# Kernel optimization log

Measured on AMD Instinct MI355X. Metric: run time of the kernel, lower is better.

Reference implementation:

```python
import jax, jax.numpy as jnp
import numpy as np
import math

B, S, HID = 2, 1024, 2048
NH, HD = 16, 128
STREAM_R, SELECT_R, RECENT_R = 0.02, 0.06, 0.08
FF = 0.9  # forgetting factor
ROPE_BASE = 10000.0


def setup_inputs() -> dict:
    key = jax.random.key(0)
    ks = jax.random.split(key, 5)
    return {
        "hidden_states": jax.random.normal(ks[0], (B, S, HID), dtype=jnp.float32),
        "wq": jax.random.normal(ks[1], (HID, HID), dtype=jnp.float32) * 0.02,
        "wk": jax.random.normal(ks[2], (HID, HID), dtype=jnp.float32) * 0.02,
        "wv": jax.random.normal(ks[3], (HID, HID), dtype=jnp.float32) * 0.02,
        "wo": jax.random.normal(ks[4], (HID, HID), dtype=jnp.float32) * 0.02,
    }


def _rope_tables(seq_len, dim):
    inv_freq = 1.0 / (ROPE_BASE ** (jnp.arange(0, dim, 2, dtype=jnp.float32) / dim))
    freqs = jnp.outer(jnp.arange(seq_len, dtype=jnp.float32), inv_freq)  # [S, D/2]
    emb = jnp.concatenate([freqs, freqs], axis=-1)  # [S, D]
    return jnp.cos(emb), jnp.sin(emb)


def _rotate_half(x):
    x1, x2 = jnp.split(x, 2, axis=-1)
    return jnp.concatenate([-x2, x1], axis=-1)


def a2s_base_mask(attn_weights, sb, selb, rb, ff):
    # attn_weights: [B,H,S,S] (causal mask already added). Returns bool keep-mask [B,H,S,S].
    Bv, Hv, Sq, Sk = attn_weights.shape
    scores = jax.nn.softmax(attn_weights.astype(jnp.float32), axis=-1)  # [B,H,S,S]
    cb = sb + selb + rb  # cache budget
    # EMA warmup over first cb rows: sum_i ff^(cb-1-i) * scores[i]
    w = ff ** jnp.arange(cb - 1, -1, -1, dtype=jnp.float32)
    select0 = jnp.einsum('t,bhts->bhs', w, scores[:, :, :cb, :])
    mask0 = jnp.ones((Bv, Hv, Sk), dtype=bool)
    pos = jnp.arange(Sk)

    xs_scores = jnp.moveaxis(scores[:, :, cb:Sk - 1, :], 2, 0)  # [T,B,H,S]
    ts = jnp.arange(cb, Sk - 1, dtype=jnp.int32)

    def step(carry, inp):
        sel, m = carry
        sc, t = inp
        cur = sc * m
        cur = cur / jnp.sum(cur, axis=-1, keepdims=True)
        sel = ff * sel + cur
        local = t - rb
        # argmin over window [sb : local+1]; outside -> +inf (evicted entries already +inf)
        win = jnp.where((pos >= sb) & (pos <= local), sel, jnp.inf)
        mi = jnp.argmin(win, axis=-1)  # [B,H], first-min like torch
        evict = pos == mi[..., None]  # [B,H,S] one-hot bool
        sel = jnp.where(evict, jnp.inf, sel)
        m_new = m & ~evict
        return (sel, m_new), m_new

    _, rows = jax.lax.scan(step, (select0, mask0), (xs_scores, ts))
    head = jnp.ones((Bv, Hv, cb + 1, Sk), dtype=bool)  # rows 0..cb stay all-True
    tail = jnp.moveaxis(rows, 0, 2)  # rows cb+1..S-1
    return jnp.concatenate([head, tail], axis=2)


def reference(hidden_states, wq, wk, wv, wo):
    sb = math.floor(STREAM_R * S + 0.5)
    selb = math.floor(SELECT_R * S + 0.5)
    rb = math.floor(RECENT_R * S + 0.5)

    q = (hidden_states @ wq).reshape(B, S, NH, HD).transpose(0, 2, 1, 3)
    k = (hidden_states @ wk).reshape(B, S, NH, HD).transpose(0, 2, 1, 3)
    v = (hidden_states @ wv).reshape(B, S, NH, HD).transpose(0, 2, 1, 3)

    cos, sin = _rope_tables(S, HD)  # [S,HD]
    q = q * cos + _rotate_half(q) * sin
    k = k * cos + _rotate_half(k) * sin

    attn = jnp.einsum('bhqd,bhkd->bhqk', q, k) / math.sqrt(HD)
    mask_val = jnp.finfo(jnp.float32).min
    causal = jnp.where(jnp.tril(jnp.ones((S, S), dtype=bool)), 0.0, mask_val)[None, None]
    attn = jnp.maximum(attn + causal, mask_val)

    keep = a2s_base_mask(jax.lax.stop_gradient(attn), sb, selb, rb, FF)
    attn = jnp.where(keep, attn, mask_val)  # torch.min(attention_mask) == mask_val

    probs = jax.nn.softmax(attn.astype(jnp.float32), axis=-1).astype(q.dtype)
    out = jnp.einsum('bhqk,bhkd->bhqd', probs, v)
    out = out.transpose(0, 2, 1, 3).reshape(B, S, HID)
    return out @ wo
```

## Files before the change

### kernel.cpp

```cpp
#include <hip/hip_runtime.h>
#include <math.h>

#define Bb    2
#define Ss    1024
#define HIDd  2048
#define NHh   16
#define HDd   128
#define SBc   20
#define SELBc 61
#define RBc   82
#define CBc   163
#define FFf   0.9f
#define MASKVAL (-3.4028234663852886e38f)
#define NBH   (Bb*NHh)
#define NROWS (NBH*Ss)

typedef __attribute__((ext_vector_type(8))) short short8;
typedef __attribute__((ext_vector_type(4))) float f32x4;

__device__ __forceinline__ unsigned short f2b(float f) {
    unsigned u = __float_as_uint(f);
    u = (u + 0x7FFFu + ((u >> 16) & 1u)) >> 16;
    return (unsigned short)u;
}
__device__ __forceinline__ float b2f(unsigned short h) {
    return __uint_as_float((unsigned)h << 16);
}

__global__ __launch_bounds__(256) void conv_split(const float* __restrict__ x,
                                                  unsigned short* __restrict__ yh,
                                                  unsigned short* __restrict__ yl, int n4)
{
    int i = blockIdx.x * 256 + threadIdx.x;
    if (i >= n4) return;
    float4 v = ((const float4*)x)[i];
    ushort4 h, l;
    h.x = f2b(v.x); l.x = f2b(v.x - b2f(h.x));
    h.y = f2b(v.y); l.y = f2b(v.y - b2f(h.y));
    h.z = f2b(v.z); l.z = f2b(v.z - b2f(h.z));
    h.w = f2b(v.w); l.w = f2b(v.w - b2f(h.w));
    ((ushort4*)yh)[i] = h;
    ((ushort4*)yl)[i] = l;
}

__global__ __launch_bounds__(256) void tconv(const float* __restrict__ W,
                                             unsigned short* __restrict__ Wt,
                                             int Kdim, int Ndim)
{
    __shared__ float T[64][65];
    int n0 = blockIdx.x * 64, k0 = blockIdx.y * 64;
    int tid = threadIdx.x;
    int rr = tid >> 4, cc = (tid & 15) * 4;
#pragma unroll
    for (int p = 0; p < 4; ++p) {
        int r = rr + p * 16;
        float4 x = *(const float4*)&W[(size_t)(k0 + r) * Ndim + n0 + cc];
        T[r][cc] = x.x; T[r][cc + 1] = x.y; T[r][cc + 2] = x.z; T[r][cc + 3] = x.w;
    }
    __syncthreads();
#pragma unroll
    for (int p = 0; p < 4; ++p) {
        int rn = rr + p * 16;
        ushort4 o;
        o.x = f2b(T[cc][rn]);     o.y = f2b(T[cc + 1][rn]);
        o.z = f2b(T[cc + 2][rn]); o.w = f2b(T[cc + 3][rn]);
        *(ushort4*)&Wt[(size_t)(n0 + rn) * Kdim + k0 + cc] = o;
    }
}

__global__ __launch_bounds__(256) void tconv_split(const float* __restrict__ W,
                                                   unsigned short* __restrict__ Wth,
                                                   unsigned short* __restrict__ Wtl,
                                                   int Kdim, int Ndim)
{
    __shared__ float T[64][65];
    int n0 = blockIdx.x * 64, k0 = blockIdx.y * 64;
    int tid = threadIdx.x;
    int rr = tid >> 4, cc = (tid & 15) * 4;
#pragma unroll
    for (int p = 0; p < 4; ++p) {
        int r = rr + p * 16;
        float4 x = *(const float4*)&W[(size_t)(k0 + r) * Ndim + n0 + cc];
        T[r][cc] = x.x; T[r][cc + 1] = x.y; T[r][cc + 2] = x.z; T[r][cc + 3] = x.w;
    }
    __syncthreads();
#pragma unroll
    for (int p = 0; p < 4; ++p) {
        int rn = rr + p * 16;
        float v0 = T[cc][rn], v1 = T[cc + 1][rn], v2 = T[cc + 2][rn], v3 = T[cc + 3][rn];
        ushort4 h, l;
        h.x = f2b(v0); l.x = f2b(v0 - b2f(h.x));
        h.y = f2b(v1); l.y = f2b(v1 - b2f(h.y));
        h.z = f2b(v2); l.z = f2b(v2 - b2f(h.z));
        h.w = f2b(v3); l.w = f2b(v3 - b2f(h.w));
        *(ushort4*)&Wth[(size_t)(n0 + rn) * Kdim + k0 + cc] = h;
        *(ushort4*)&Wtl[(size_t)(n0 + rn) * Kdim + k0 + cc] = l;
    }
}

template<int MODE>
__global__ __launch_bounds__(256) void gemm_bf16t(const unsigned short* __restrict__ A,
                                                  const unsigned short* __restrict__ Bt,
                                                  float* __restrict__ C,
                                                  int M, int N, int K)
{
    __shared__ unsigned short As[128 * 32];
    __shared__ unsigned short Bs[128 * 32];
    const int tid = threadIdx.x;
    const int bm = blockIdx.y * 128, bn = blockIdx.x * 128;
    const int lane = tid & 63, wid = tid >> 6;
    const int wr = (wid >> 1) * 64, wc = (wid & 1) * 64;
    const int lm = lane & 15, lk = (lane >> 4) * 8;

    f32x4 acc[4][4];
#pragma unroll
    for (int mi = 0; mi < 4; ++mi)
#pragma unroll
        for (int ni = 0; ni < 4; ++ni) acc[mi][ni] = 0.0f;

    for (int k0 = 0; k0 < K; k0 += 32) {
#pragma unroll
        for (int l = 0; l < 2; ++l) {
            int L = tid + l * 256;
            int row = L >> 2, c8 = (L & 3) * 8;
            *(short8*)&As[row * 32 + c8] = *(const short8*)&A[(size_t)(bm + row) * K + k0 + c8];
            *(short8*)&Bs[row * 32 + c8] = *(const short8*)&Bt[(size_t)(bn + row) * K + k0 + c8];
        }
        __syncthreads();
        short8 af[4], bf[4];
#pragma unroll
        for (int mi = 0; mi < 4; ++mi) af[mi] = *(short8*)&As[(wr + mi * 16 + lm) * 32 + lk];
#pragma unroll
        for (int ni = 0; ni < 4; ++ni) bf[ni] = *(short8*)&Bs[(wc + ni * 16 + lm) * 32 + lk];
#pragma unroll
        for (int mi = 0; mi < 4; ++mi)
#pragma unroll
            for (int ni = 0; ni < 4; ++ni)
                acc[mi][ni] = __builtin_amdgcn_mfma_f32_16x16x32_bf16(af[mi], bf[ni], acc[mi][ni], 0, 0, 0);
        __syncthreads();
    }
    const int lr = (lane >> 4) * 4;
#pragma unroll
    for (int mi = 0; mi < 4; ++mi)
#pragma unroll
        for (int ni = 0; ni < 4; ++ni)
#pragma unroll
            for (int r = 0; r < 4; ++r) {
                int m = bm + wr + mi * 16 + lr + r;
                int n = bn + wc + ni * 16 + lm;
                float vv = acc[mi][ni][r];
                if (MODE == 0) {
                    C[(size_t)m * N + n] = vv;
                } else {
                    int b_ = m / Ss, s_ = m % Ss;
                    int h_ = n / HDd, d_ = n % HDd;
                    C[(size_t)((b_ * NHh + h_) * Ss + s_) * HDd + d_] = vv;
                }
            }
}

template<int MODE>
__global__ __launch_bounds__(256) void gemm_split(const unsigned short* __restrict__ Ah,
                                                  const unsigned short* __restrict__ Al,
                                                  const unsigned short* __restrict__ Bh,
                                                  const unsigned short* __restrict__ Bl,
                                                  float* __restrict__ C,
                                                  int M, int N, int K)
{
    __shared__ unsigned short AsH[128 * 32], AsL[128 * 32];
    __shared__ unsigned short BsH[128 * 32], BsL[128 * 32];
    const int tid = threadIdx.x;
    const int bm = blockIdx.y * 128, bn = blockIdx.x * 128;
    const int lane = tid & 63, wid = tid >> 6;
    const int wr = (wid >> 1) * 64, wc = (wid & 1) * 64;
    const int lm = lane & 15, lk = (lane >> 4) * 8;

    f32x4 acc[4][4];
#pragma unroll
    for (int mi = 0; mi < 4; ++mi)
#pragma unroll
        for (int ni = 0; ni < 4; ++ni) acc[mi][ni] = 0.0f;

    for (int k0 = 0; k0 < K; k0 += 32) {
#pragma unroll
        for (int l = 0; l < 2; ++l) {
            int L = tid + l * 256;
            int row = L >> 2, c8 = (L & 3) * 8;
            size_t ga = (size_t)(bm + row) * K + k0 + c8;
            size_t gb = (size_t)(bn + row) * K + k0 + c8;
            *(short8*)&AsH[row * 32 + c8] = *(const short8*)&Ah[ga];
            *(short8*)&AsL[row * 32 + c8] = *(const short8*)&Al[ga];
            *(short8*)&BsH[row * 32 + c8] = *(const short8*)&Bh[gb];
            *(short8*)&BsL[row * 32 + c8] = *(const short8*)&Bl[gb];
        }
        __syncthreads();
        short8 ah[4], al[4], bh[4], bl[4];
#pragma unroll
        for (int mi = 0; mi < 4; ++mi) {
            ah[mi] = *(short8*)&AsH[(wr + mi * 16 + lm) * 32 + lk];
            al[mi] = *(short8*)&AsL[(wr + mi * 16 + lm) * 32 + lk];
        }
#pragma unroll
        for (int ni = 0; ni < 4; ++ni) {
            bh[ni] = *(short8*)&BsH[(wc + ni * 16 + lm) * 32 + lk];
            bl[ni] = *(short8*)&BsL[(wc + ni * 16 + lm) * 32 + lk];
        }
#pragma unroll
        for (int mi = 0; mi < 4; ++mi)
#pragma unroll
            for (int ni = 0; ni < 4; ++ni) {
                acc[mi][ni] = __builtin_amdgcn_mfma_f32_16x16x32_bf16(ah[mi], bh[ni], acc[mi][ni], 0, 0, 0);
                acc[mi][ni] = __builtin_amdgcn_mfma_f32_16x16x32_bf16(ah[mi], bl[ni], acc[mi][ni], 0, 0, 0);
                acc[mi][ni] = __builtin_amdgcn_mfma_f32_16x16x32_bf16(al[mi], bh[ni], acc[mi][ni], 0, 0, 0);
            }
        __syncthreads();
    }
    const int lr = (lane >> 4) * 4;
#pragma unroll
    for (int mi = 0; mi < 4; ++mi)
#pragma unroll
        for (int ni = 0; ni < 4; ++ni)
#pragma unroll
            for (int r = 0; r < 4; ++r) {
                int m = bm + wr + mi * 16 + lr + r;
                int n = bn + wc + ni * 16 + lm;
                float vv = acc[mi][ni][r];
                if (MODE == 0) {
                    C[(size_t)m * N + n] = vv;
                } else {
                    int b_ = m / Ss, s_ = m % Ss;
                    int h_ = n / HDd, d_ = n % HDd;
                    C[(size_t)((b_ * NHh + h_) * Ss + s_) * HDd + d_] = vv;
                }
            }
}

__global__ __launch_bounds__(64) void rope_qk_split(const float* __restrict__ q,
                                                    const float* __restrict__ k,
                                                    unsigned short* __restrict__ qh,
                                                    unsigned short* __restrict__ ql,
                                                    unsigned short* __restrict__ kh,
                                                    unsigned short* __restrict__ kl)
{
    int idx = blockIdx.x;
    int s = idx % Ss;
    int d = threadIdx.x;
    float inv = powf(10000.0f, -2.0f * (float)d / 128.0f);
    float fr = (float)s * inv;
    float c = cosf(fr), sn = sinf(fr);
    size_t base = (size_t)idx * HDd;
    float q1 = q[base + d], q2 = q[base + d + 64];
    float k1 = k[base + d], k2 = k[base + d + 64];
    float qa = q1 * c - q2 * sn, qbv = q2 * c + q1 * sn;
    float ka = k1 * c - k2 * sn, kbv = k2 * c + k1 * sn;
    unsigned short h;
    h = f2b(qa);  qh[base + d]      = h; ql[base + d]      = f2b(qa  - b2f(h));
    h = f2b(qbv); qh[base + d + 64] = h; ql[base + d + 64] = f2b(qbv - b2f(h));
    h = f2b(ka);  kh[base + d]      = h; kl[base + d]      = f2b(ka  - b2f(h));
    h = f2b(kbv); kh[base + d + 64] = h; kl[base + d + 64] = f2b(kbv - b2f(h));
}

__global__ __launch_bounds__(256) void attn_qk_split(const unsigned short* __restrict__ qh,
                                                     const unsigned short* __restrict__ ql,
                                                     const unsigned short* __restrict__ kh,
                                                     const unsigned short* __restrict__ kl,
                                                     float* __restrict__ attn)
{
    const int bh = blockIdx.z;
    const int bm = blockIdx.y * 128, bn = blockIdx.x * 128;
    float* C = attn + (size_t)bh * Ss * Ss;
    const int tid = threadIdx.x;

    if (blockIdx.x > blockIdx.y) {
        float4 mv = make_float4(MASKVAL, MASKVAL, MASKVAL, MASKVAL);
#pragma unroll
        for (int i = 0; i < 16; ++i) {
            int L = tid + i * 256;
            int row = L >> 5, c4 = (L & 31) * 4;
            *(float4*)&C[(size_t)(bm + row) * Ss + bn + c4] = mv;
        }
        return;
    }
    const size_t hb = (size_t)bh * Ss * HDd;
    const unsigned short* Ah = qh + hb;
    const unsigned short* Al = ql + hb;
    const unsigned short* Bh = kh + hb;
    const unsigned short* Bl = kl + hb;

    __shared__ unsigned short AsH[128 * 32], AsL[128 * 32];
    __shared__ unsigned short BsH[128 * 32], BsL[128 * 32];
    const int lane = tid & 63, wid = tid >> 6;
    const int wr = (wid >> 1) * 64, wc = (wid & 1) * 64;
    const int lm = lane & 15, lk = (lane >> 4) * 8;

    f32x4 acc[4][4];
#pragma unroll
    for (int mi = 0; mi < 4; ++mi)
#pragma unroll
        for (int ni = 0; ni < 4; ++ni) acc[mi][ni] = 0.0f;

    for (int k0 = 0; k0 < HDd; k0 += 32) {
#pragma unroll
        for (int l = 0; l < 2; ++l) {
            int L = tid + l * 256;
            int row = L >> 2, c8 = (L & 3) * 8;
            size_t ga = (size_t)(bm + row) * HDd + k0 + c8;
            size_t gb = (size_t)(bn + row) * HDd + k0 + c8;
            *(short8*)&AsH[row * 32 + c8] = *(const short8*)&Ah[ga];
            *(short8*)&AsL[row * 32 + c8] = *(const short8*)&Al[ga];
            *(short8*)&BsH[row * 32 + c8] = *(const short8*)&Bh[gb];
            *(short8*)&BsL[row * 32 + c8] = *(const short8*)&Bl[gb];
        }
        __syncthreads();
        short8 ah[4], al[4], bh2[4], bl2[4];
#pragma unroll
        for (int mi = 0; mi < 4; ++mi) {
            ah[mi] = *(short8*)&AsH[(wr + mi * 16 + lm) * 32 + lk];
            al[mi] = *(short8*)&AsL[(wr + mi * 16 + lm) * 32 + lk];
        }
#pragma unroll
        for (int ni = 0; ni < 4; ++ni) {
            bh2[ni] = *(short8*)&BsH[(wc + ni * 16 + lm) * 32 + lk];
            bl2[ni] = *(short8*)&BsL[(wc + ni * 16 + lm) * 32 + lk];
        }
#pragma unroll
        for (int mi = 0; mi < 4; ++mi)
#pragma unroll
            for (int ni = 0; ni < 4; ++ni) {
                acc[mi][ni] = __builtin_amdgcn_mfma_f32_16x16x32_bf16(ah[mi], bh2[ni], acc[mi][ni], 0, 0, 0);
                acc[mi][ni] = __builtin_amdgcn_mfma_f32_16x16x32_bf16(ah[mi], bl2[ni], acc[mi][ni], 0, 0, 0);
                acc[mi][ni] = __builtin_amdgcn_mfma_f32_16x16x32_bf16(al[mi], bh2[ni], acc[mi][ni], 0, 0, 0);
            }
        __syncthreads();
    }
    const float scale = 0.08838834764831845f;
    const int lr = (lane >> 4) * 4;
#pragma unroll
    for (int mi = 0; mi < 4; ++mi)
#pragma unroll
        for (int ni = 0; ni < 4; ++ni)
#pragma unroll
            for (int r = 0; r < 4; ++r) {
                int sq = bm + wr + mi * 16 + lr + r;
                int sk = bn + wc + ni * 16 + lm;
                C[(size_t)sq * Ss + sk] = (sk <= sq) ? acc[mi][ni][r] * scale : MASKVAL;
            }
}

__global__ __launch_bounds__(256) void softmax_rows(float* __restrict__ attn)
{
    int row = blockIdx.x;
    float4* a4 = (float4*)(attn + (size_t)row * Ss);
    int tid = threadIdx.x;
    float4 x = a4[tid];
    float m = fmaxf(fmaxf(x.x, x.y), fmaxf(x.z, x.w));
#pragma unroll
    for (int off = 32; off; off >>= 1) m = fmaxf(m, __shfl_xor(m, off));
    __shared__ float red[4];
    if ((tid & 63) == 0) red[tid >> 6] = m;
    __syncthreads();
    float mm = fmaxf(fmaxf(red[0], red[1]), fmaxf(red[2], red[3]));
    float e0 = expf(x.x - mm), e1 = expf(x.y - mm);
    float e2 = expf(x.z - mm), e3 = expf(x.w - mm);
    float s = e0 + e1 + e2 + e3;
#pragma unroll
    for (int off = 32; off; off >>= 1) s += __shfl_xor(s, off);
    __shared__ float red2[4];
    if ((tid & 63) == 0) red2[tid >> 6] = s;
    __syncthreads();
    float inv = 1.0f / (red2[0] + red2[1] + red2[2] + red2[3]);
    a4[tid] = make_float4(e0 * inv, e1 * inv, e2 * inv, e3 * inv);
}

template<int CTRL>
__device__ __forceinline__ int dpp_i(int x) {
    return __builtin_amdgcn_update_dpp(0, x, CTRL, 0xF, 0xF, true);
}
__device__ __forceinline__ float wave_sum64(float x) {
    x += __int_as_float(dpp_i<0xB1>(__float_as_int(x)));
    x += __int_as_float(dpp_i<0x4E>(__float_as_int(x)));
    x += __int_as_float(dpp_i<0x141>(__float_as_int(x)));
    x += __int_as_float(dpp_i<0x140>(__float_as_int(x)));
    int xi = __float_as_int(x);
    float a = __int_as_float(__builtin_amdgcn_readlane(xi, 0));
    float b = __int_as_float(__builtin_amdgcn_readlane(xi, 16));
    float c = __int_as_float(__builtin_amdgcn_readlane(xi, 32));
    float d = __int_as_float(__builtin_amdgcn_readlane(xi, 48));
    return (a + c) + (b + d);
}

__device__ __forceinline__ unsigned long long u64min(unsigned long long a, unsigned long long b) {
    return a < b ? a : b;
}
template<int CTRL>
__device__ __forceinline__ unsigned long long dpp64(unsigned long long x) {
    int lo = (int)(unsigned)x;
    int hi = (int)(unsigned)(x >> 32);
    unsigned l2 = (unsigned)dpp_i<CTRL>(lo);
    unsigned h2 = (unsigned)dpp_i<CTRL>(hi);
    return ((unsigned long long)h2 << 32) | (unsigned long long)l2;
}
__device__ __forceinline__ unsigned long long wave_min64k(unsigned long long x) {
    x = u64min(x, dpp64<0xB1>(x));
    x = u64min(x, dpp64<0x4E>(x));
    x = u64min(x, dpp64<0x141>(x));
    x = u64min(x, dpp64<0x140>(x));
    int lo = (int)(unsigned)x;
    int hi = (int)(unsigned)(x >> 32);
    unsigned long long a = ((unsigned long long)(unsigned)__builtin_amdgcn_readlane(hi, 0)  << 32) |
                           (unsigned long long)(unsigned)__builtin_amdgcn_readlane(lo, 0);
    unsigned long long b = ((unsigned long long)(unsigned)__builtin_amdgcn_readlane(hi, 16) << 32) |
                           (unsigned long long)(unsigned)__builtin_amdgcn_readlane(lo, 16);
    unsigned long long c = ((unsigned long long)(unsigned)__builtin_amdgcn_readlane(hi, 32) << 32) |
                           (unsigned long long)(unsigned)__builtin_amdgcn_readlane(lo, 32);
    unsigned long long d = ((unsigned long long)(unsigned)__builtin_amdgcn_readlane(hi, 48) << 32) |
                           (unsigned long long)(unsigned)__builtin_amdgcn_readlane(lo, 48);
    return u64min(u64min(a, b), u64min(c, d));
}

__device__ __forceinline__ float f4c(float4 v, int i) {
    return i == 0 ? v.x : (i == 1 ? v.y : (i == 2 ? v.z : v.w));
}

template<int NC, int NCL>
__device__ __forceinline__ void scan_step(int t, int lane,
                                          const float4* __restrict__ A4,
                                          unsigned char* __restrict__ KP,
                                          float4 (&rb)[4],
                                          float (&sel)[4][4],
                                          float (&mf)[4][4])
{
    const float INFv = __int_as_float(0x7f800000);
    float4 a[NC];
#pragma unroll
    for (int jj = 0; jj < NC; ++jj) a[jj] = rb[jj];
    int tp = t + 4; if (tp > Ss - 1) tp = Ss - 1;
#pragma unroll
    for (int jj = 0; jj < NCL; ++jj) rb[jj] = A4[tp * 256 + jj * 64 + lane];

    float lsum = 0.0f;
#pragma unroll
    for (int jj = 0; jj < NC; ++jj) {
        float c0 = a[jj].x * mf[jj][0], c1 = a[jj].y * mf[jj][1];
        float c2 = a[jj].z * mf[jj][2], c3 = a[jj].w * mf[jj][3];
        lsum += (c0 + c1) + (c2 + c3);
    }
    float tot = wave_sum64(lsum);
    float inv = 1.0f / tot;

    const int local = t - RBc;
    const int base = lane * 4;
    const bool ge = (base >= SBc);

    unsigned long long kmin = 0xFFFFFFFFFFFFFFFFull;
#pragma unroll
    for (int jj = 0; jj < NC; ++jj) {
        unsigned long long kk[4];
#pragma unroll
        for (int i = 0; i < 4; ++i) {
            float sv = fmaf(FFf, sel[jj][i], f4c(a[jj], i) * inv);
            sel[jj][i] = sv;
            int s = jj * 256 + base + i;
            bool win = (s <= local) && (jj > 0 || ge);
            unsigned hi = win ? __float_as_uint(sv) : 0x7f800000u;
            kk[i] = ((unsigned long long)hi << 32) | (unsigned long long)(unsigned)s;
        }
        unsigned long long cm = u64min(u64min(kk[0], kk[1]), u64min(kk[2], kk[3]));
        kmin = u64min(kmin, cm);
    }
    kmin = wave_min64k(kmin);
    const int besti = (int)(unsigned)(kmin & 0xFFFFFFFFull);

#pragma unroll
    for (int jj = 0; jj < NC; ++jj)
#pragma unroll
        for (int i = 0; i < 4; ++i) {
            int s = jj * 256 + base + i;
            bool e = (s == besti);
            sel[jj][i] = e ? INFv : sel[jj][i];
            mf[jj][i]  = e ? 0.0f : mf[jj][i];
        }

    uchar4* kp4 = (uchar4*)(KP + (size_t)(t + 1) * Ss);
#pragma unroll
    for (int jj = 0; jj < NC; ++jj) {
        uchar4 kb;
        kb.x = (unsigned char)mf[jj][0];
        kb.y = (unsigned char)mf[jj][1];
        kb.z = (unsigned char)mf[jj][2];
        kb.w = (unsigned char)mf[jj][3];
        kp4[jj * 64 + lane] = kb;
    }
}

__global__ __launch_bounds__(64) void scan_kernel5(const float* __restrict__ scores,
                                                   unsigned char* __restrict__ keep)
{
    int bh = blockIdx.x;
    int lane = threadIdx.x;
    const float4* A4 = (const float4*)(scores + (size_t)bh * Ss * Ss);
    unsigned char* KP = keep + (size_t)bh * Ss * Ss;

    float sel[4][4];
    float mf[4][4];
#pragma unroll
    for (int jj = 0; jj < 4; ++jj)
#pragma unroll
        for (int i = 0; i < 4; ++i) { sel[jj][i] = 0.0f; mf[jj][i] = 1.0f; }

    float4 w0 = A4[0 * 256 + lane];
    float4 w1 = A4[1 * 256 + lane];
    float4 w2 = A4[2 * 256 + lane];
    float4 w3 = A4[3 * 256 + lane];
#define WSTEP(W, NEXT)                                                       \
    do {                                                                     \
        float4 _a = W;                                                       \
        W = A4[(NEXT) * 256 + lane];                                         \
        sel[0][0] = fmaf(FFf, sel[0][0], _a.x);                              \
        sel[0][1] = fmaf(FFf, sel[0][1], _a.y);                              \
        sel[0][2] = fmaf(FFf, sel[0][2], _a.z);                              \
        sel[0][3] = fmaf(FFf, sel[0][3], _a.w);                              \
    } while (0)
    for (int r = 0; r < 160; r += 4) {
        WSTEP(w0, r + 4); WSTEP(w1, r + 5); WSTEP(w2, r + 6); WSTEP(w3, r + 7);
    }
#undef WSTEP
    {
        float4 tl[3] = { w0, w1, w2 };
#pragma unroll
        for (int u = 0; u < 3; ++u) {
            sel[0][0] = fmaf(FFf, sel[0][0], tl[u].x);
            sel[0][1] = fmaf(FFf, sel[0][1], tl[u].y);
            sel[0][2] = fmaf(FFf, sel[0][2], tl[u].z);
            sel[0][3] = fmaf(FFf, sel[0][3], tl[u].w);
        }
    }

    float4 rb[4][4];
#pragma unroll
    for (int slot = 0; slot < 4; ++slot)
        rb[slot][0] = A4[(163 + slot) * 256 + lane];

    for (int t0 = 163; t0 < 255; t0 += 4) {
        scan_step<1, 2>(t0 + 0, lane, A4, KP, rb[0], sel, mf);
        scan_step<1, 2>(t0 + 1, lane, A4, KP, rb[1], sel, mf);
        scan_step<1, 2>(t0 + 2, lane, A4, KP, rb[2], sel, mf);
        scan_step<1, 2>(t0 + 3, lane, A4, KP, rb[3], sel, mf);
    }
    for (int t0 = 255; t0 < 511; t0 += 4) {
        scan_step<2, 3>(t0 + 0, lane, A4, KP, rb[0], sel, mf);
        scan_step<2, 3>(t0 + 1, lane, A4, KP, rb[1], sel, mf);
        scan_step<2, 3>(t0 + 2, lane, A4, KP, rb[2], sel, mf);
        scan_step<2, 3>(t0 + 3, lane, A4, KP, rb[3], sel, mf);
    }
    for (int t0 = 511; t0 < 767; t0 += 4) {
        scan_step<3, 4>(t0 + 0, lane, A4, KP, rb[0], sel, mf);
        scan_step<3, 4>(t0 + 1, lane, A4, KP, rb[1], sel, mf);
        scan_step<3, 4>(t0 + 2, lane, A4, KP, rb[2], sel, mf);
        scan_step<3, 4>(t0 + 3, lane, A4, KP, rb[3], sel, mf);
    }
    for (int t0 = 767; t0 < 1023; t0 += 4) {
        scan_step<4, 4>(t0 + 0, lane, A4, KP, rb[0], sel, mf);
        scan_step<4, 4>(t0 + 1, lane, A4, KP, rb[1], sel, mf);
        scan_step<4, 4>(t0 + 2, lane, A4, KP, rb[2], sel, mf);
        scan_step<4, 4>(t0 + 3, lane, A4, KP, rb[3], sel, mf);
    }
}

__global__ __launch_bounds__(256) void renorm_rows(float* __restrict__ scores,
                                                   const unsigned char* __restrict__ keep)
{
    int row = blockIdx.x;
    int r = row % Ss;
    float4* a4 = (float4*)(scores + (size_t)row * Ss);
    int tid = threadIdx.x;
    float4 x = a4[tid];
    if (r > CBc) {
        const uchar4* kp = (const uchar4*)(keep + (size_t)row * Ss);
        uchar4 kb = kp[tid];
        if (!kb.x) x.x = 0.0f;
        if (!kb.y) x.y = 0.0f;
        if (!kb.z) x.z = 0.0f;
        if (!kb.w) x.w = 0.0f;
    }
    float s = (x.x + x.y) + (x.z + x.w);
#pragma unroll
    for (int off = 32; off; off >>= 1) s += __shfl_xor(s, off);
    __shared__ float red2[4];
    if ((tid & 63) == 0) red2[tid >> 6] = s;
    __syncthreads();
    float inv = 1.0f / (red2[0] + red2[1] + red2[2] + red2[3]);
    a4[tid] = make_float4(x.x * inv, x.y * inv, x.z * inv, x.w * inv);
}

__global__ __launch_bounds__(256) void pv_gemm(const float* __restrict__ probs,
                                               const float* __restrict__ v,
                                               unsigned short* __restrict__ ctxb)
{
    int bh = blockIdx.z;
    int b_ = bh / NHh, h_ = bh % NHh;
    const float* P = probs + (size_t)bh * Ss * Ss;
    const float* V = v     + (size_t)bh * Ss * HDd;
    int bm = blockIdx.y * 64, bn = blockIdx.x * 64;
    int tid = threadIdx.x, tx = tid & 15, ty = tid >> 4;
    __shared__ float As[16][65];
    __shared__ float Bs[16][64];
    float acc[4][4] = {};
    int kend = bm + 64;
    for (int k0 = 0; k0 < kend; k0 += 16) {
#pragma unroll
        for (int l = 0; l < 4; ++l) {
            int idx = tid + l * 256;
            int r = idx >> 4, c = idx & 15;
            As[c][r] = P[(size_t)(bm + r) * Ss + k0 + c];
        }
#pragma unroll
        for (int l = 0; l < 4; ++l) {
            int idx = tid + l * 256;
            int r = idx >> 6, c = idx & 63;
            Bs[r][c] = V[(size_t)(k0 + r) * HDd + bn + c];
        }
        __syncthreads();
#pragma unroll
        for (int kk = 0; kk < 16; ++kk) {
            float a[4], b[4];
#pragma unroll
            for (int i = 0; i < 4; ++i) a[i] = As[kk][ty * 4 + i];
#pragma unroll
            for (int j = 0; j < 4; ++j) b[j] = Bs[kk][tx * 4 + j];
#pragma unroll
            for (int i = 0; i < 4; ++i)
#pragma unroll
                for (int j = 0; j < 4; ++j)
                    acc[i][j] = fmaf(a[i], b[j], acc[i][j]);
        }
        __syncthreads();
    }
#pragma unroll
    for (int i = 0; i < 4; ++i) {
        int sq = bm + ty * 4 + i;
#pragma unroll
        for (int j = 0; j < 4; ++j) {
            int d = bn + tx * 4 + j;
            ctxb[(size_t)(b_ * Ss + sq) * HIDd + h_ * HDd + d] = f2b(acc[i][j]);
        }
    }
}

extern "C" void kernel_launch(void* const* d_in, const int* in_sizes, int n_in,
                              void* d_out, int out_size, void* d_ws, size_t ws_size,
                              hipStream_t stream)
{
    const float* hs = (const float*)d_in[0];
    const float* wq = (const float*)d_in[1];
    const float* wk = (const float*)d_in[2];
    const float* wv = (const float*)d_in[3];
    const float* wo = (const float*)d_in[4];
    float* out = (float*)d_out;

    float* ws = (float*)d_ws;
    size_t off = 0;
    float* qf   = ws + off; off += (size_t)NBH * Ss * HDd;
    float* kf   = ws + off; off += (size_t)NBH * Ss * HDd;
    float* vf   = ws + off; off += (size_t)NBH * Ss * HDd;
    float* attn = ws + off; off += (size_t)NBH * Ss * Ss;
    unsigned char* keep = (unsigned char*)(ws + off); off += (size_t)NBH * Ss * Ss / 4;
    unsigned short* wot = (unsigned short*)(ws + off); off += (size_t)HIDd * HIDd / 2;

    unsigned short* hsh  = (unsigned short*)(attn);
    unsigned short* hsl  = (unsigned short*)(attn + 2u * 1024 * 1024);
    unsigned short* wqth = (unsigned short*)(attn + 4u * 1024 * 1024);
    unsigned short* wqtl = (unsigned short*)(attn + 6u * 1024 * 1024);
    unsigned short* wkth = (unsigned short*)(attn + 8u * 1024 * 1024);
    unsigned short* wktl = (unsigned short*)(attn + 10u * 1024 * 1024);
    unsigned short* wvt  = (unsigned short*)(attn + 12u * 1024 * 1024);
    unsigned short* qh = (unsigned short*)keep;
    unsigned short* ql = (unsigned short*)(keep + 8u * 1024 * 1024);
    unsigned short* kh = (unsigned short*)(keep + 16u * 1024 * 1024);
    unsigned short* kl = (unsigned short*)(keep + 24u * 1024 * 1024);
    unsigned short* ctxb = (unsigned short*)qf;

    dim3 blk(256);
    const int M = Bb * Ss;

    conv_split<<<dim3((M * HIDd / 4 + 255) / 256), blk, 0, stream>>>(hs, hsh, hsl, M * HIDd / 4);

    dim3 gt(HIDd / 64, HIDd / 64);
    tconv_split<<<gt, blk, 0, stream>>>(wq, wqth, wqtl, HIDd, HIDd);
    tconv_split<<<gt, blk, 0, stream>>>(wk, wkth, wktl, HIDd, HIDd);
    tconv<<<gt, blk, 0, stream>>>(wv, wvt, HIDd, HIDd);
    tconv<<<gt, blk, 0, stream>>>(wo, wot, HIDd, HIDd);

    dim3 gp(HIDd / 128, M / 128);
    gemm_split<1><<<gp, blk, 0, stream>>>(hsh, hsl, wqth, wqtl, qf, M, HIDd, HIDd);
    gemm_split<1><<<gp, blk, 0, stream>>>(hsh, hsl, wkth, wktl, kf, M, HIDd, HIDd);
    gemm_bf16t<1><<<gp, blk, 0, stream>>>(hsh, wvt, vf, M, HIDd, HIDd);

    rope_qk_split<<<dim3(NBH * Ss), dim3(64), 0, stream>>>(qf, kf, qh, ql, kh, kl);

    attn_qk_split<<<dim3(Ss / 128, Ss / 128, NBH), blk, 0, stream>>>(qh, ql, kh, kl, attn);

    softmax_rows<<<dim3(NROWS), blk, 0, stream>>>(attn);

    scan_kernel5<<<dim3(NBH), dim3(64), 0, stream>>>(attn, keep);

    renorm_rows<<<dim3(NROWS), blk, 0, stream>>>(attn, keep);

    pv_gemm<<<dim3(HDd / 64, Ss / 64, NBH), blk, 0, stream>>>(attn, vf, ctxb);

    gemm_bf16t<0><<<gp, blk, 0, stream>>>(ctxb, wot, out, M, HIDd, HIDd);
}
```

Measured before the change: 1.040 ms.

## Fuse weight conversions, merge QKV GEMMs, fold renorm into PV, use direct LDS loads

Merges the four weight transpose/convert kernels into one launch and the Q, K and V projections into one grid. The upper-triangle mask fill in QK^T is dropped, and softmax now reads only the causal prefix of each row. The separate renorm pass is folded into the PV GEMM, which masks evicted keys on load and divides by the accumulated row sum. Tile loads switch to global_load_lds when the builtin is available. These target launch overhead and redundant passes over the S×S score matrix, with the risk that downstream code relies on the masked upper region no longer being written.

```diff
diff --git a/kernel.cpp b/kernel.cpp
--- a/kernel.cpp
+++ b/kernel.cpp
@@ -27,6 +27,22 @@
     return __uint_as_float((unsigned)h << 16);
 }
 
+#if defined(__has_builtin)
+#if __has_builtin(__builtin_amdgcn_global_load_lds)
+#define USE_GLD 1
+#endif
+#endif
+
+__device__ __forceinline__ void gload16(const void* g, void* l) {
+#ifdef USE_GLD
+    __builtin_amdgcn_global_load_lds(
+        (const __attribute__((address_space(1))) void*)g,
+        (__attribute__((address_space(3))) void*)l, 16, 0, 0);
+#else
+    *(short8*)l = *(const short8*)g;
+#endif
+}
+
 __global__ __launch_bounds__(256) void conv_split(const float* __restrict__ x,
                                                   unsigned short* __restrict__ yh,
                                                   unsigned short* __restrict__ yl, int n4)
@@ -43,62 +59,174 @@
     ((ushort4*)yl)[i] = l;
 }
 
-__global__ __launch_bounds__(256) void tconv(const float* __restrict__ W,
-                                             unsigned short* __restrict__ Wt,
-                                             int Kdim, int Ndim)
+__global__ __launch_bounds__(256) void tconv_all(const float* __restrict__ wq,
+                                                 const float* __restrict__ wk,
+                                                 const float* __restrict__ wv,
+                                                 const float* __restrict__ wo,
+                                                 unsigned short* __restrict__ wqth,
+                                                 unsigned short* __restrict__ wqtl,
+                                                 unsigned short* __restrict__ wkth,
+                                                 unsigned short* __restrict__ wktl,
+                                                 unsigned short* __restrict__ wvt,
+                                                 unsigned short* __restrict__ wot)
 {
     __shared__ float T[64][65];
+    const int z = blockIdx.z;
+    const float* W = (z == 0) ? wq : (z == 1) ? wk : (z == 2) ? wv : wo;
     int n0 = blockIdx.x * 64, k0 = blockIdx.y * 64;
     int tid = threadIdx.x;
     int rr = tid >> 4, cc = (tid & 15) * 4;
 #pragma unroll
     for (int p = 0; p < 4; ++p) {
         int r = rr + p * 16;
-        float4 x = *(const float4*)&W[(size_t)(k0 + r) * Ndim + n0 + cc];
+        float4 x = *(const float4*)&W[(size_t)(k0 + r) * HIDd + n0 + cc];
         T[r][cc] = x.x; T[r][cc + 1] = x.y; T[r][cc + 2] = x.z; T[r][cc + 3] = x.w;
     }
     __syncthreads();
-#pragma unroll
-    for (int p = 0; p < 4; ++p) {
-        int rn = rr + p * 16;
-        ushort4 o;
-        o.x = f2b(T[cc][rn]);     o.y = f2b(T[cc + 1][rn]);
-        o.z = f2b(T[cc + 2][rn]); o.w = f2b(T[cc + 3][rn]);
-        *(ushort4*)&Wt[(size_t)(n0 + rn) * Kdim + k0 + cc] = o;
-    }
-}
-
-__global__ __launch_bounds__(256) void tconv_split(const float* __restrict__ W,
-                                                   unsigned short* __restrict__ Wth,
-                                                   unsigned short* __restrict__ Wtl,
-                                                   int Kdim, int Ndim)
-{
-    __shared__ float T[64][65];
-    int n0 = blockIdx.x * 64, k0 = blockIdx.y * 64;
-    int tid = threadIdx.x;
-    int rr = tid >> 4, cc = (tid & 15) * 4;
-#pragma unroll
-    for (int p = 0; p < 4; ++p) {
-        int r = rr + p * 16;
-        float4 x = *(const float4*)&W[(size_t)(k0 + r) * Ndim + n0 + cc];
-        T[r][cc] = x.x; T[r][cc + 1] = x.y; T[r][cc + 2] = x.z; T[r][cc + 3] = x.w;
-    }
-    __syncthreads();
-#pragma unroll
-    for (int p = 0; p < 4; ++p) {
-        int rn = rr + p * 16;
-        float v0 = T[cc][rn], v1 = T[cc + 1][rn], v2 = T[cc + 2][rn], v3 = T[cc + 3][rn];
-        ushort4 h, l;
-        h.x = f2b(v0); l.x = f2b(v0 - b2f(h.x));
-        h.y = f2b(v1); l.y = f2b(v1 - b2f(h.y));
-        h.z = f2b(v2); l.z = f2b(v2 - b2f(h.z));
-        h.w = f2b(v3); l.w = f2b(v3 - b2f(h.w));
-        *(ushort4*)&Wth[(size_t)(n0 + rn) * Kdim + k0 + cc] = h;
-        *(ushort4*)&Wtl[(size_t)(n0 + rn) * Kdim + k0 + cc] = l;
-    }
-}
-
-template<int MODE>
+    if (z < 2) {
+        unsigned short* Wth = z ? wkth : wqth;
+        unsigned short* Wtl = z ? wktl : wqtl;
+#pragma unroll
+        for (int p = 0; p < 4; ++p) {
+            int rn = rr + p * 16;
+            float v0 = T[cc][rn], v1 = T[cc + 1][rn], v2 = T[cc + 2][rn], v3 = T[cc + 3][rn];
+            ushort4 h, l;
+            h.x = f2b(v0); l.x = f2b(v0 - b2f(h.x));
+            h.y = f2b(v1); l.y = f2b(v1 - b2f(h.y));
+            h.z = f2b(v2); l.z = f2b(v2 - b2f(h.z));
+            h.w = f2b(v3); l.w = f2b(v3 - b2f(h.w));
+            *(ushort4*)&Wth[(size_t)(n0 + rn) * HIDd + k0 + cc] = h;
+            *(ushort4*)&Wtl[(size_t)(n0 + rn) * HIDd + k0 + cc] = l;
+        }
+    } else {
+        unsigned short* Wt = (z == 2) ? wvt : wot;
+#pragma unroll
+        for (int p = 0; p < 4; ++p) {
+            int rn = rr + p * 16;
+            ushort4 o;
+            o.x = f2b(T[cc][rn]);     o.y = f2b(T[cc + 1][rn]);
+            o.z = f2b(T[cc + 2][rn]); o.w = f2b(T[cc + 3][rn]);
+            *(ushort4*)&Wt[(size_t)(n0 + rn) * HIDd + k0 + cc] = o;
+        }
+    }
+}
+
+__global__ __launch_bounds__(256) void gemm_qkv(const unsigned short* __restrict__ hsh,
+                                                const unsigned short* __restrict__ hsl,
+                                                const unsigned short* __restrict__ wqth,
+                                                const unsigned short* __restrict__ wqtl,
+                                                const unsigned short* __restrict__ wkth,
+                                                const unsigned short* __restrict__ wktl,
+                                                const unsigned short* __restrict__ wvt,
+                                                float* __restrict__ qf,
+                                                float* __restrict__ kf,
+                                                float* __restrict__ vf)
+{
+    __shared__ unsigned short AsH[128 * 32], AsL[128 * 32];
+    __shared__ unsigned short BsH[128 * 32], BsL[128 * 32];
+    const int tid = threadIdx.x;
+    const int region = blockIdx.x >> 4;
+    const int bn = (blockIdx.x & 15) * 128;
+    const int bm = blockIdx.y * 128;
+    const int K = HIDd;
+    const int lane = tid & 63, wid = tid >> 6;
+    const int wr = (wid >> 1) * 64, wc = (wid & 1) * 64;
+    const int lm = lane & 15, lk = (lane >> 4) * 8;
+    const int lr = (lane >> 4) * 4;
+
+    f32x4 acc[4][4];
+#pragma unroll
+    for (int mi = 0; mi < 4; ++mi)
+#pragma unroll
+        for (int ni = 0; ni < 4; ++ni) acc[mi][ni] = 0.0f;
+
+    if (region < 2) {
+        const unsigned short* Bh = region ? wkth : wqth;
+        const unsigned short* Bl = region ? wktl : wqtl;
+        float* C = region ? kf : qf;
+        for (int k0 = 0; k0 < K; k0 += 32) {
+#pragma unroll
+            for (int l = 0; l < 2; ++l) {
+                int L = tid + l * 256;
+                int row = L >> 2, c8 = (L & 3) * 8;
+                size_t ga = (size_t)(bm + row) * K + k0 + c8;
+                size_t gb = (size_t)(bn + row) * K + k0 + c8;
+                gload16(&hsh[ga], &AsH[L * 8]);
+                gload16(&hsl[ga], &AsL[L * 8]);
+                gload16(&Bh[gb], &BsH[L * 8]);
+                gload16(&Bl[gb], &BsL[L * 8]);
+            }
+            __syncthreads();
+            short8 ah[4], al[4], bh[4], bl[4];
+#pragma unroll
+            for (int mi = 0; mi < 4; ++mi) {
+                ah[mi] = *(short8*)&AsH[(wr + mi * 16 + lm) * 32 + lk];
+                al[mi] = *(short8*)&AsL[(wr + mi * 16 + lm) * 32 + lk];
+            }
+#pragma unroll
+            for (int ni = 0; ni < 4; ++ni) {
+                bh[ni] = *(short8*)&BsH[(wc + ni * 16 + lm) * 32 + lk];
+                bl[ni] = *(short8*)&BsL[(wc + ni * 16 + lm) * 32 + lk];
+            }
+#pragma unroll
+            for (int mi = 0; mi < 4; ++mi)
+#pragma unroll
+                for (int ni = 0; ni < 4; ++ni) {
+                    acc[mi][ni] = __builtin_amdgcn_mfma_f32_16x16x32_bf16(ah[mi], bh[ni], acc[mi][ni], 0, 0, 0);
+                    acc[mi][ni] = __builtin_amdgcn_mfma_f32_16x16x32_bf16(ah[mi], bl[ni], acc[mi][ni], 0, 0, 0);
+                    acc[mi][ni] = __builtin_amdgcn_mfma_f32_16x16x32_bf16(al[mi], bh[ni], acc[mi][ni], 0, 0, 0);
+                }
+            __syncthreads();
+        }
+#pragma unroll
+        for (int mi = 0; mi < 4; ++mi)
+#pragma unroll
+            for (int ni = 0; ni < 4; ++ni)
+#pragma unroll
+                for (int r = 0; r < 4; ++r) {
+                    int m = bm + wr + mi * 16 + lr + r;
+                    int n = bn + wc + ni * 16 + lm;
+                    int b_ = m / Ss, s_ = m % Ss;
+                    int h_ = n / HDd, d_ = n % HDd;
+                    C[(size_t)((b_ * NHh + h_) * Ss + s_) * HDd + d_] = acc[mi][ni][r];
+                }
+    } else {
+        for (int k0 = 0; k0 < K; k0 += 32) {
+#pragma unroll
+            for (int l = 0; l < 2; ++l) {
+                int L = tid + l * 256;
+                int row = L >> 2, c8 = (L & 3) * 8;
+                gload16(&hsh[(size_t)(bm + row) * K + k0 + c8], &AsH[L * 8]);
+                gload16(&wvt[(size_t)(bn + row) * K + k0 + c8], &BsH[L * 8]);
+            }
+            __syncthreads();
+            short8 af[4], bf[4];
+#pragma unroll
+            for (int mi = 0; mi < 4; ++mi) af[mi] = *(short8*)&AsH[(wr + mi * 16 + lm) * 32 + lk];
+#pragma unroll
+            for (int ni = 0; ni < 4; ++ni) bf[ni] = *(short8*)&BsH[(wc + ni * 16 + lm) * 32 + lk];
+#pragma unroll
+            for (int mi = 0; mi < 4; ++mi)
+#pragma unroll
+                for (int ni = 0; ni < 4; ++ni)
+                    acc[mi][ni] = __builtin_amdgcn_mfma_f32_16x16x32_bf16(af[mi], bf[ni], acc[mi][ni], 0, 0, 0);
+            __syncthreads();
+        }
+#pragma unroll
+        for (int mi = 0; mi < 4; ++mi)
+#pragma unroll
+            for (int ni = 0; ni < 4; ++ni)
+#pragma unroll
+                for (int r = 0; r < 4; ++r) {
+                    int m = bm + wr + mi * 16 + lr + r;
+                    int n = bn + wc + ni * 16 + lm;
+                    int b_ = m / Ss, s_ = m % Ss;
+                    int h_ = n / HDd, d_ = n % HDd;
+                    vf[(size_t)((b_ * NHh + h_) * Ss + s_) * HDd + d_] = acc[mi][ni][r];
+                }
+    }
+}
+
 __global__ __launch_bounds__(256) void gemm_bf16t(const unsigned short* __restrict__ A,
                                                   const unsigned short* __restrict__ Bt,
                                                   float* __restrict__ C,
@@ -123,8 +251,8 @@
         for (int l = 0; l < 2; ++l) {
             int L = tid + l * 256;
             int row = L >> 2, c8 = (L & 3) * 8;
-            *(short8*)&As[row * 32 + c8] = *(const short8*)&A[(size_t)(bm + row) * K + k0 + c8];
-            *(short8*)&Bs[row * 32 + c8] = *(const short8*)&Bt[(size_t)(bn + row) * K + k0 + c8];
+            gload16(&A[(size_t)(bm + row) * K + k0 + c8], &As[L * 8]);
+            gload16(&Bt[(size_t)(bn + row) * K + k0 + c8], &Bs[L * 8]);
         }
         __syncthreads();
         short8 af[4], bf[4];
@@ -148,90 +276,7 @@
             for (int r = 0; r < 4; ++r) {
                 int m = bm + wr + mi * 16 + lr + r;
                 int n = bn + wc + ni * 16 + lm;
-                float vv = acc[mi][ni][r];
-                if (MODE == 0) {
-                    C[(size_t)m * N + n] = vv;
-                } else {
-                    int b_ = m / Ss, s_ = m % Ss;
-                    int h_ = n / HDd, d_ = n % HDd;
-                    C[(size_t)((b_ * NHh + h_) * Ss + s_) * HDd + d_] = vv;
-                }
-            }
-}
-
-template<int MODE>
-__global__ __launch_bounds__(256) void gemm_split(const unsigned short* __restrict__ Ah,
-                                                  const unsigned short* __restrict__ Al,
-                                                  const unsigned short* __restrict__ Bh,
-                                                  const unsigned short* __restrict__ Bl,
-                                                  float* __restrict__ C,
-                                                  int M, int N, int K)
-{
-    __shared__ unsigned short AsH[128 * 32], AsL[128 * 32];
-    __shared__ unsigned short BsH[128 * 32], BsL[128 * 32];
-    const int tid = threadIdx.x;
-    const int bm = blockIdx.y * 128, bn = blockIdx.x * 128;
-    const int lane = tid & 63, wid = tid >> 6;
-    const int wr = (wid >> 1) * 64, wc = (wid & 1) * 64;
-    const int lm = lane & 15, lk = (lane >> 4) * 8;
-
-    f32x4 acc[4][4];
-#pragma unroll
-    for (int mi = 0; mi < 4; ++mi)
-#pragma unroll
-        for (int ni = 0; ni < 4; ++ni) acc[mi][ni] = 0.0f;
-
-    for (int k0 = 0; k0 < K; k0 += 32) {
-#pragma unroll
-        for (int l = 0; l < 2; ++l) {
-            int L = tid + l * 256;
-            int row = L >> 2, c8 = (L & 3) * 8;
-            size_t ga = (size_t)(bm + row) * K + k0 + c8;
-            size_t gb = (size_t)(bn + row) * K + k0 + c8;
-            *(short8*)&AsH[row * 32 + c8] = *(const short8*)&Ah[ga];
-            *(short8*)&AsL[row * 32 + c8] = *(const short8*)&Al[ga];
-            *(short8*)&BsH[row * 32 + c8] = *(const short8*)&Bh[gb];
-            *(short8*)&BsL[row * 32 + c8] = *(const short8*)&Bl[gb];
-        }
-        __syncthreads();
-        short8 ah[4], al[4], bh[4], bl[4];
-#pragma unroll
-        for (int mi = 0; mi < 4; ++mi) {
-            ah[mi] = *(short8*)&AsH[(wr + mi * 16 + lm) * 32 + lk];
-            al[mi] = *(short8*)&AsL[(wr + mi * 16 + lm) * 32 + lk];
-        }
-#pragma unroll
-        for (int ni = 0; ni < 4; ++ni) {
-            bh[ni] = *(short8*)&BsH[(wc + ni * 16 + lm) * 32 + lk];
-            bl[ni] = *(short8*)&BsL[(wc + ni * 16 + lm) * 32 + lk];
-        }
-#pragma unroll
-        for (int mi = 0; mi < 4; ++mi)
-#pragma unroll
-            for (int ni = 0; ni < 4; ++ni) {
-                acc[mi][ni] = __builtin_amdgcn_mfma_f32_16x16x32_bf16(ah[mi], bh[ni], acc[mi][ni], 0, 0, 0);
-                acc[mi][ni] = __builtin_amdgcn_mfma_f32_16x16x32_bf16(ah[mi], bl[ni], acc[mi][ni], 0, 0, 0);
-                acc[mi][ni] = __builtin_amdgcn_mfma_f32_16x16x32_bf16(al[mi], bh[ni], acc[mi][ni], 0, 0, 0);
-            }
-        __syncthreads();
-    }
-    const int lr = (lane >> 4) * 4;
-#pragma unroll
-    for (int mi = 0; mi < 4; ++mi)
-#pragma unroll
-        for (int ni = 0; ni < 4; ++ni)
-#pragma unroll
-            for (int r = 0; r < 4; ++r) {
-                int m = bm + wr + mi * 16 + lr + r;
-                int n = bn + wc + ni * 16 + lm;
-                float vv = acc[mi][ni][r];
-                if (MODE == 0) {
-                    C[(size_t)m * N + n] = vv;
-                } else {
-                    int b_ = m / Ss, s_ = m % Ss;
-                    int h_ = n / HDd, d_ = n % HDd;
-                    C[(size_t)((b_ * NHh + h_) * Ss + s_) * HDd + d_] = vv;
-                }
+                C[(size_t)m * N + n] = acc[mi][ni][r];
             }
 }
 
@@ -271,16 +316,8 @@
     float* C = attn + (size_t)bh * Ss * Ss;
     const int tid = threadIdx.x;
 
-    if (blockIdx.x > blockIdx.y) {
-        float4 mv = make_float4(MASKVAL, MASKVAL, MASKVAL, MASKVAL);
-#pragma unroll
-        for (int i = 0; i < 16; ++i) {
-            int L = tid + i * 256;
-            int row = L >> 5, c4 = (L & 31) * 4;
-            *(float4*)&C[(size_t)(bm + row) * Ss + bn + c4] = mv;
-        }
-        return;
-    }
+    if (blockIdx.x > blockIdx.y) return;
+
     const size_t hb = (size_t)bh * Ss * HDd;
     const unsigned short* Ah = qh + hb;
     const unsigned short* Al = ql + hb;
@@ -306,10 +343,10 @@
             int row = L >> 2, c8 = (L & 3) * 8;
             size_t ga = (size_t)(bm + row) * HDd + k0 + c8;
             size_t gb = (size_t)(bn + row) * HDd + k0 + c8;
-            *(short8*)&AsH[row * 32 + c8] = *(const short8*)&Ah[ga];
-            *(short8*)&AsL[row * 32 + c8] = *(const short8*)&Al[ga];
-            *(short8*)&BsH[row * 32 + c8] = *(const short8*)&Bh[gb];
-            *(short8*)&BsL[row * 32 + c8] = *(const short8*)&Bl[gb];
+            gload16(&Ah[ga], &AsH[L * 8]);
+            gload16(&Al[ga], &AsL[L * 8]);
+            gload16(&Bh[gb], &BsH[L * 8]);
+            gload16(&Bl[gb], &BsL[L * 8]);
         }
         __syncthreads();
         short8 ah[4], al[4], bh2[4], bl2[4];
@@ -350,9 +387,12 @@
 __global__ __launch_bounds__(256) void softmax_rows(float* __restrict__ attn)
 {
     int row = blockIdx.x;
+    int r = row & (Ss - 1);
     float4* a4 = (float4*)(attn + (size_t)row * Ss);
     int tid = threadIdx.x;
-    float4 x = a4[tid];
+    bool act = (tid * 4 <= r);
+    float4 x = make_float4(MASKVAL, MASKVAL, MASKVAL, MASKVAL);
+    if (act) x = a4[tid];
     float m = fmaxf(fmaxf(x.x, x.y), fmaxf(x.z, x.w));
 #pragma unroll
     for (int off = 32; off; off >>= 1) m = fmaxf(m, __shfl_xor(m, off));
@@ -567,52 +607,32 @@
     }
 }
 
-__global__ __launch_bounds__(256) void renorm_rows(float* __restrict__ scores,
-                                                   const unsigned char* __restrict__ keep)
-{
-    int row = blockIdx.x;
-    int r = row % Ss;
-    float4* a4 = (float4*)(scores + (size_t)row * Ss);
-    int tid = threadIdx.x;
-    float4 x = a4[tid];
-    if (r > CBc) {
-        const uchar4* kp = (const uchar4*)(keep + (size_t)row * Ss);
-        uchar4 kb = kp[tid];
-        if (!kb.x) x.x = 0.0f;
-        if (!kb.y) x.y = 0.0f;
-        if (!kb.z) x.z = 0.0f;
-        if (!kb.w) x.w = 0.0f;
-    }
-    float s = (x.x + x.y) + (x.z + x.w);
-#pragma unroll
-    for (int off = 32; off; off >>= 1) s += __shfl_xor(s, off);
-    __shared__ float red2[4];
-    if ((tid & 63) == 0) red2[tid >> 6] = s;
-    __syncthreads();
-    float inv = 1.0f / (red2[0] + red2[1] + red2[2] + red2[3]);
-    a4[tid] = make_float4(x.x * inv, x.y * inv, x.z * inv, x.w * inv);
-}
-
-__global__ __launch_bounds__(256) void pv_gemm(const float* __restrict__ probs,
-                                               const float* __restrict__ v,
-                                               unsigned short* __restrict__ ctxb)
+__global__ __launch_bounds__(256) void pv_renorm(const float* __restrict__ scores,
+                                                 const unsigned char* __restrict__ keep,
+                                                 const float* __restrict__ v,
+                                                 unsigned short* __restrict__ ctxb)
 {
     int bh = blockIdx.z;
     int b_ = bh / NHh, h_ = bh % NHh;
-    const float* P = probs + (size_t)bh * Ss * Ss;
-    const float* V = v     + (size_t)bh * Ss * HDd;
+    const float* P = scores + (size_t)bh * Ss * Ss;
+    const unsigned char* KPm = keep + (size_t)bh * Ss * Ss;
+    const float* V = v + (size_t)bh * Ss * HDd;
     int bm = blockIdx.y * 64, bn = blockIdx.x * 64;
     int tid = threadIdx.x, tx = tid & 15, ty = tid >> 4;
     __shared__ float As[16][65];
     __shared__ float Bs[16][64];
     float acc[4][4] = {};
+    float rs[4] = {};
     int kend = bm + 64;
     for (int k0 = 0; k0 < kend; k0 += 16) {
 #pragma unroll
         for (int l = 0; l < 4; ++l) {
             int idx = tid + l * 256;
             int r = idx >> 4, c = idx & 15;
-            As[c][r] = P[(size_t)(bm + r) * Ss + k0 + c];
+            int row = bm + r;
+            float p = P[(size_t)row * Ss + k0 + c];
+            if (row > CBc && !KPm[(size_t)row * Ss + k0 + c]) p = 0.0f;
+            As[c][r] = p;
         }
 #pragma unroll
         for (int l = 0; l < 4; ++l) {
@@ -629,6 +649,8 @@
 #pragma unroll
             for (int j = 0; j < 4; ++j) b[j] = Bs[kk][tx * 4 + j];
 #pragma unroll
+            for (int i = 0; i < 4; ++i) rs[i] += a[i];
+#pragma unroll
             for (int i = 0; i < 4; ++i)
 #pragma unroll
                 for (int j = 0; j < 4; ++j)
@@ -638,11 +660,12 @@
     }
 #pragma unroll
     for (int i = 0; i < 4; ++i) {
+        float inv = 1.0f / rs[i];
         int sq = bm + ty * 4 + i;
 #pragma unroll
         for (int j = 0; j < 4; ++j) {
             int d = bn + tx * 4 + j;
-            ctxb[(size_t)(b_ * Ss + sq) * HIDd + h_ * HDd + d] = f2b(acc[i][j]);
+            ctxb[(size_t)(b_ * Ss + sq) * HIDd + h_ * HDd + d] = f2b(acc[i][j] * inv);
         }
     }
 }
@@ -685,16 +708,11 @@
 
     conv_split<<<dim3((M * HIDd / 4 + 255) / 256), blk, 0, stream>>>(hs, hsh, hsl, M * HIDd / 4);
 
-    dim3 gt(HIDd / 64, HIDd / 64);
-    tconv_split<<<gt, blk, 0, stream>>>(wq, wqth, wqtl, HIDd, HIDd);
-    tconv_split<<<gt, blk, 0, stream>>>(wk, wkth, wktl, HIDd, HIDd);
-    tconv<<<gt, blk, 0, stream>>>(wv, wvt, HIDd, HIDd);
-    tconv<<<gt, blk, 0, stream>>>(wo, wot, HIDd, HIDd);
-
-    dim3 gp(HIDd / 128, M / 128);
-    gemm_split<1><<<gp, blk, 0, stream>>>(hsh, hsl, wqth, wqtl, qf, M, HIDd, HIDd);
-    gemm_split<1><<<gp, blk, 0, stream>>>(hsh, hsl, wkth, wktl, kf, M, HIDd, HIDd);
-    gemm_bf16t<1><<<gp, blk, 0, stream>>>(hsh, wvt, vf, M, HIDd, HIDd);
+    tconv_all<<<dim3(HIDd / 64, HIDd / 64, 4), blk, 0, stream>>>(
+        wq, wk, wv, wo, wqth, wqtl, wkth, wktl, wvt, wot);
+
+    gemm_qkv<<<dim3(48, M / 128), blk, 0, stream>>>(
+        hsh, hsl, wqth, wqtl, wkth, wktl, wvt, qf, kf, vf);
 
     rope_qk_split<<<dim3(NBH * Ss), dim3(64), 0, stream>>>(qf, kf, qh, ql, kh, kl);
 
@@ -704,9 +722,7 @@
 
     scan_kernel5<<<dim3(NBH), dim3(64), 0, stream>>>(attn, keep);
 
-    renorm_rows<<<dim3(NROWS), blk, 0, stream>>>(attn, keep);
-
-    pv_gemm<<<dim3(HDd / 64, Ss / 64, NBH), blk, 0, stream>>>(attn, vf, ctxb);
-
-    gemm_bf16t<0><<<gp, blk, 0, stream>>>(ctxb, wot, out, M, HIDd, HIDd);
-}
+    pv_renorm<<<dim3(HDd / 64, Ss / 64, NBH), blk, 0, stream>>>(attn, keep, vf, ctxb);
+
+    gemm_bf16t<<<dim3(HIDd / 128, M / 128), blk, 0, stream>>>(ctxb, wot, out, M, HIDd, HIDd);
+}
```

Result: faster. 985.9 us (-5.2%).
